# Performance work log

Measured on AMD Instinct MI355X. Metric: run time of the kernel, lower is better.

The kernel has to match this reference:

```python
import jax, jax.numpy as jnp
import numpy as np

HIDDEN = 256
HEADS = 8
HEAD_DIM = HIDDEN // HEADS
BATCH = 2
N_NODES = 8192
N_EDGES = 262144


def setup_inputs() -> dict:
    key = jax.random.key(0)
    ks = jax.random.split(key, 12)
    node_states = jax.random.normal(ks[0], (BATCH, N_NODES, HIDDEN), dtype=jnp.float32)
    b_idx = jax.random.randint(ks[1], (N_EDGES,), 0, BATCH)
    s_idx = jax.random.randint(ks[2], (N_EDGES,), 0, N_NODES)
    t_idx = jax.random.randint(ks[3], (N_EDGES,), 0, N_NODES)
    edge_indices = jnp.stack([b_idx, s_idx, t_idx]).astype(jnp.int64)
    edge_values = jax.random.normal(ks[4], (N_EDGES, HIDDEN), dtype=jnp.float32)
    scale = 1.0 / np.sqrt(HIDDEN)
    Wq = jax.random.normal(ks[5], (HIDDEN, HIDDEN), dtype=jnp.float32) * scale
    bq = jnp.zeros((HIDDEN,), jnp.float32)
    Wk = jax.random.normal(ks[6], (HIDDEN, HIDDEN), dtype=jnp.float32) * scale
    bk = jnp.zeros((HIDDEN,), jnp.float32)
    Wv = jax.random.normal(ks[7], (HIDDEN, HIDDEN), dtype=jnp.float32) * scale
    bv = jnp.zeros((HIDDEN,), jnp.float32)
    We = jax.random.normal(ks[8], (HIDDEN, HIDDEN), dtype=jnp.float32) * scale
    be = jnp.zeros((HIDDEN,), jnp.float32)
    return {"node_states": node_states, "edge_indices": edge_indices, "edge_values": edge_values,
            "Wq": Wq, "bq": bq, "Wk": Wk, "bk": bk, "Wv": Wv, "bv": bv, "We": We, "be": be}


def reference(node_states, edge_indices, edge_values, Wq, bq, Wk, bk, Wv, bv, We, be):
    batch, n_nodes, hidden = node_states.shape
    E = edge_indices.shape[1]
    b_idx, s_idx, t_idx = edge_indices[0], edge_indices[1], edge_indices[2]

    # Dense QKV projections over nodes (torch Linear: x @ W.T + b)
    Q = node_states @ Wq.T + bq
    K = node_states @ Wk.T + bk
    V = node_states @ Wv.T + bv

    # Gather per-edge query/key/value, split heads -> (E, H, D)
    Qm = Q[b_idx, s_idx].reshape(E, HEADS, HEAD_DIM)
    Kn = K[b_idx, t_idx].reshape(E, HEADS, HEAD_DIM)
    Vn = V[b_idx, t_idx].reshape(E, HEADS, HEAD_DIM)

    # Edge feature projections (use_edge_values=True path)
    Ke = (edge_values @ Wk.T + bk).reshape(E, HEADS, HEAD_DIM)
    Ve = (edge_values @ We.T + be).reshape(E, HEADS, HEAD_DIM)

    inv_sqrt_d = 1.0 / jnp.sqrt(jnp.float32(HEAD_DIM))
    # node2node + node2edge = Qm.(Kn+Ke)/sqrt(d)  -> (E, H)
    logits = jnp.sum(Qm * (Kn + Ke), axis=-1) * inv_sqrt_d

    # torch.sparse.softmax(..., dim=-1): dim -1 of (B,N,N,H) is the DENSE heads
    # dim, so softmax is taken over the heads axis of the per-edge values.
    attn = jax.nn.softmax(logits, axis=-1)  # (E, H)

    out_edges = (attn[..., None] * (Vn + Ve)).reshape(E, hidden)  # (E, hidden)

    # Scatter-sum edges to their (batch, src) node: sparse.mm with 0/1 mask
    seg = b_idx * n_nodes + s_idx
    flat = jax.ops.segment_sum(out_edges, seg, num_segments=batch * n_nodes)
    return flat.reshape(batch, n_nodes, hidden)
```

## Files before the change

### kernel.cpp

```cpp
#include <hip/hip_runtime.h>
#include <hip/hip_bf16.h>

#define HID 256
#define NN 8192
#define NE 262144

typedef float f32x4 __attribute__((ext_vector_type(4)));
typedef __bf16 bf16x8 __attribute__((ext_vector_type(8)));
typedef __bf16 bf16x4 __attribute__((ext_vector_type(4)));

__global__ void conv_weights(const float* __restrict__ wq, const float* __restrict__ wk,
                             const float* __restrict__ wv, const float* __restrict__ we,
                             __bf16* __restrict__ o) {
    int i = blockIdx.x * 256 + threadIdx.x;
    const float* srcs[4] = {wq, wk, wv, we};
    int m = i >> 16;
    int j = i & 65535;
    o[i] = (__bf16)srcs[m][j];
}

__global__ __launch_bounds__(256, 6)
void qkv_gemm(const float* __restrict__ x,
              const __bf16* __restrict__ wbf,
              const float* __restrict__ bq, const float* __restrict__ bk,
              const float* __restrict__ bv,
              __bf16* __restrict__ qbf, __bf16* __restrict__ kbf,
              __bf16* __restrict__ vbf) {
    __shared__ __bf16 xt[32 * 256];
    char* lb = (char*)xt;
    int tid = threadIdx.x;
    int blk = blockIdx.x;
    int m = blockIdx.y;

    const float4* xs = (const float4*)(x + (size_t)blk * 32 * 256);
    #pragma unroll
    for (int kq = 0; kq < 8; ++kq) {
        int f = tid + kq * 256;
        int row = f >> 6, c4 = f & 63;
        float4 v = xs[f];
        bf16x4 h;
        h[0] = (__bf16)v.x; h[1] = (__bf16)v.y; h[2] = (__bf16)v.z; h[3] = (__bf16)v.w;
        int off = (row * 512 + c4 * 8) ^ ((row & 7) << 4);
        *(bf16x4*)(lb + off) = h;
    }
    __syncthreads();

    int w = tid >> 6, lane = tid & 63;
    int l15 = lane & 15, l4 = lane >> 4;
    int cw = w * 64;
    const float* bias = (m == 0) ? bq : ((m == 1) ? bk : bv);
    __bf16* out = (m == 0) ? qbf : ((m == 1) ? kbf : vbf);

    const __bf16* W = wbf + (size_t)m * 65536;
    f32x4 acc[4][2] = {};
    for (int ks = 0; ks < 8; ++ks) {
        bf16x8 aW[4], bE[2];
        #pragma unroll
        for (int tn = 0; tn < 4; ++tn)
            aW[tn] = *(const bf16x8*)(W + (size_t)(cw + tn * 16 + l15) * 256 + ks * 32 + l4 * 8);
        #pragma unroll
        for (int te = 0; te < 2; ++te) {
            int row = te * 16 + l15;
            int off = (row * 512 + ks * 64 + l4 * 16) ^ ((row & 7) << 4);
            bE[te] = *(const bf16x8*)(lb + off);
        }
        #pragma unroll
        for (int tn = 0; tn < 4; ++tn)
            #pragma unroll
            for (int te = 0; te < 2; ++te)
                acc[tn][te] = __builtin_amdgcn_mfma_f32_16x16x32_bf16(aW[tn], bE[te], acc[tn][te], 0, 0, 0);
    }
    #pragma unroll
    for (int tn = 0; tn < 4; ++tn) {
        float4 b4 = *(const float4*)(bias + cw + tn * 16 + l4 * 4);
        #pragma unroll
        for (int te = 0; te < 2; ++te) {
            int row = blk * 32 + te * 16 + l15;
            int col = cw + tn * 16 + l4 * 4;
            bf16x4 h;
            h[0] = (__bf16)(acc[tn][te][0] + b4.x);
            h[1] = (__bf16)(acc[tn][te][1] + b4.y);
            h[2] = (__bf16)(acc[tn][te][2] + b4.z);
            h[3] = (__bf16)(acc[tn][te][3] + b4.w);
            *(bf16x4*)(out + (size_t)row * 256 + col) = h;
        }
    }
}

__global__ void k_hist(const int* __restrict__ eidx, unsigned* __restrict__ hist) {
    int e = blockIdx.x * 256 + threadIdx.x;
    int key = eidx[e] * NN + eidx[NE + e];
    atomicAdd(&hist[key], 1u);
}

__global__ void k_scan(const unsigned* __restrict__ hist, unsigned* __restrict__ cursor) {
    __shared__ unsigned tot[256];
    int tid = threadIdx.x;
    unsigned s = 0;
    for (int i = 0; i < 64; ++i) s += hist[tid * 64 + i];
    tot[tid] = s;
    __syncthreads();
    for (int d = 1; d < 256; d <<= 1) {
        unsigned v = (tid >= d) ? tot[tid - d] : 0u;
        __syncthreads();
        tot[tid] += v;
        __syncthreads();
    }
    unsigned run = (tid == 0) ? 0u : tot[tid - 1];
    for (int i = 0; i < 64; ++i) {
        int idx = tid * 64 + i;
        cursor[idx] = run;
        run += hist[idx];
    }
}

__global__ void k_perm(const int* __restrict__ eidx, unsigned* __restrict__ cursor,
                       int* __restrict__ perm) {
    int e = blockIdx.x * 256 + threadIdx.x;
    int key = eidx[e] * NN + eidx[NE + e];
    unsigned pos = atomicAdd(&cursor[key], 1u);
    perm[pos] = e;
}

__global__ __launch_bounds__(512, 8)
void edge_logits(const float* __restrict__ ev,
                 const int* __restrict__ eidx,
                 const __bf16* __restrict__ wbf,
                 const float* __restrict__ bkb,
                 const __bf16* __restrict__ qbf, const __bf16* __restrict__ kbf,
                 float* __restrict__ attn_ws) {
    __shared__ __bf16 evt[64 * 256];
    __shared__ int sb[64], ss[64], st[64];
    char* lb = (char*)evt;
    int tid = threadIdx.x;
    int e0 = blockIdx.x * 64;

    const float4* xs = (const float4*)(ev + (size_t)e0 * 256);
    #pragma unroll
    for (int kq = 0; kq < 8; ++kq) {
        int f = tid + kq * 512;
        int row = f >> 6, c4 = f & 63;
        float4 v = xs[f];
        bf16x4 h;
        h[0] = (__bf16)v.x; h[1] = (__bf16)v.y; h[2] = (__bf16)v.z; h[3] = (__bf16)v.w;
        int off = (row * 512 + c4 * 8) ^ ((row & 7) << 4);
        *(bf16x4*)(lb + off) = h;
    }
    if (tid < 64) {
        sb[tid] = eidx[e0 + tid];
        ss[tid] = eidx[NE + e0 + tid];
        st[tid] = eidx[2 * NE + e0 + tid];
    }
    __syncthreads();

    int w = tid >> 6, lane = tid & 63;
    int l15 = lane & 15, l4 = lane >> 4;
    int cw = w * 32;

    const __bf16* WK = wbf + 65536;
    f32x4 acc[2][4] = {};
    for (int ks = 0; ks < 8; ++ks) {
        bf16x8 aW[2], bE[4];
        #pragma unroll
        for (int tn = 0; tn < 2; ++tn)
            aW[tn] = *(const bf16x8*)(WK + (size_t)(cw + tn * 16 + l15) * 256 + ks * 32 + l4 * 8);
        #pragma unroll
        for (int te = 0; te < 4; ++te) {
            int row = te * 16 + l15;
            int off = (row * 512 + ks * 64 + l4 * 16) ^ ((row & 7) << 4);
            bE[te] = *(const bf16x8*)(lb + off);
        }
        #pragma unroll
        for (int tn = 0; tn < 2; ++tn)
            #pragma unroll
            for (int te = 0; te < 4; ++te)
                acc[tn][te] = __builtin_amdgcn_mfma_f32_16x16x32_bf16(aW[tn], bE[te], acc[tn][te], 0, 0, 0);
    }
    __syncthreads();

    #pragma unroll
    for (int tn = 0; tn < 2; ++tn) {
        float4 b4 = *(const float4*)(bkb + cw + tn * 16 + l4 * 4);
        #pragma unroll
        for (int te = 0; te < 4; ++te) {
            int edge = te * 16 + l15;
            int colb = (cw + tn * 16 + l4 * 4) * 2;
            bf16x4 h;
            h[0] = (__bf16)(acc[tn][te][0] + b4.x);
            h[1] = (__bf16)(acc[tn][te][1] + b4.y);
            h[2] = (__bf16)(acc[tn][te][2] + b4.z);
            h[3] = (__bf16)(acc[tn][te][3] + b4.w);
            int off = (edge * 512 + colb) ^ ((edge & 7) << 4);
            *(bf16x4*)(lb + off) = h;
        }
    }
    __syncthreads();

    int cl = lane & 31, eh = lane >> 5;
    #pragma unroll
    for (int it = 0; it < 4; ++it) {
        int e = w * 8 + it * 2 + eh;
        int b_ = sb[e], s_ = ss[e], t_ = st[e];
        bf16x8 qv = *(const bf16x8*)(qbf + ((size_t)b_ * NN + s_) * 256 + cl * 8);
        bf16x8 kv = *(const bf16x8*)(kbf + ((size_t)b_ * NN + t_) * 256 + cl * 8);
        int off = (e * 512 + cl * 16) ^ ((e & 7) << 4);
        bf16x8 kev = *(const bf16x8*)(lb + off);
        float val = 0.f;
        #pragma unroll
        for (int j = 0; j < 8; ++j)
            val += (float)qv[j] * ((float)kv[j] + (float)kev[j]);
        val += __shfl_xor(val, 1);
        val += __shfl_xor(val, 2);
        val *= 0.17677669529663687f;
        float mx = val;
        mx = fmaxf(mx, __shfl_xor(mx, 4));
        mx = fmaxf(mx, __shfl_xor(mx, 8));
        mx = fmaxf(mx, __shfl_xor(mx, 16));
        float ex = __expf(val - mx);
        float s4 = ex;
        s4 += __shfl_xor(s4, 4);
        s4 += __shfl_xor(s4, 8);
        s4 += __shfl_xor(s4, 16);
        float a = ex / s4;
        if ((cl & 3) == 0)
            attn_ws[(size_t)(e0 + e) * 8 + (cl >> 2)] = a;
    }
}

__global__ __launch_bounds__(512, 8)
void edge_scatter2(const float* __restrict__ ev,
                   const int* __restrict__ eidx,
                   const __bf16* __restrict__ wbf,
                   const float* __restrict__ beb,
                   const __bf16* __restrict__ vbf,
                   const float* __restrict__ attn_ws,
                   const int* __restrict__ perm,
                   float* __restrict__ out) {
    __shared__ __bf16 evt[64 * 256];
    __shared__ int pe[64], sb[64], ss[64], st[64];
    char* lb = (char*)evt;
    int tid = threadIdx.x;
    int p0 = blockIdx.x * 64;

    if (tid < 64) {
        int e = perm[p0 + tid];
        pe[tid] = e;
        sb[tid] = eidx[e];
        ss[tid] = eidx[NE + e];
        st[tid] = eidx[2 * NE + e];
    }
    __syncthreads();

    #pragma unroll
    for (int kq = 0; kq < 8; ++kq) {
        int f = tid + kq * 512;
        int row = f >> 6, c4 = f & 63;
        const float4* src = (const float4*)(ev + (size_t)pe[row] * 256);
        float4 v = src[c4];
        bf16x4 h;
        h[0] = (__bf16)v.x; h[1] = (__bf16)v.y; h[2] = (__bf16)v.z; h[3] = (__bf16)v.w;
        int off = (row * 512 + c4 * 8) ^ ((row & 7) << 4);
        *(bf16x4*)(lb + off) = h;
    }
    __syncthreads();

    int w = tid >> 6, lane = tid & 63;
    int l15 = lane & 15, l4 = lane >> 4;
    int cw = w * 32;

    const __bf16* WE = wbf + 3 * 65536;
    f32x4 acc[2][4] = {};
    for (int ks = 0; ks < 8; ++ks) {
        bf16x8 aW[2], bE[4];
        #pragma unroll
        for (int tn = 0; tn < 2; ++tn)
            aW[tn] = *(const bf16x8*)(WE + (size_t)(cw + tn * 16 + l15) * 256 + ks * 32 + l4 * 8);
        #pragma unroll
        for (int te = 0; te < 4; ++te) {
            int row = te * 16 + l15;
            int off = (row * 512 + ks * 64 + l4 * 16) ^ ((row & 7) << 4);
            bE[te] = *(const bf16x8*)(lb + off);
        }
        #pragma unroll
        for (int tn = 0; tn < 2; ++tn)
            #pragma unroll
            for (int te = 0; te < 4; ++te)
                acc[tn][te] = __builtin_amdgcn_mfma_f32_16x16x32_bf16(aW[tn], bE[te], acc[tn][te], 0, 0, 0);
    }
    __syncthreads();

    #pragma unroll
    for (int tn = 0; tn < 2; ++tn) {
        float4 b4 = *(const float4*)(beb + cw + tn * 16 + l4 * 4);
        #pragma unroll
        for (int te = 0; te < 4; ++te) {
            int edge = te * 16 + l15;
            int colb = (cw + tn * 16 + l4 * 4) * 2;
            bf16x4 h;
            h[0] = (__bf16)(acc[tn][te][0] + b4.x);
            h[1] = (__bf16)(acc[tn][te][1] + b4.y);
            h[2] = (__bf16)(acc[tn][te][2] + b4.z);
            h[3] = (__bf16)(acc[tn][te][3] + b4.w);
            int off = (edge * 512 + colb) ^ ((edge & 7) << 4);
            *(bf16x4*)(lb + off) = h;
        }
    }
    __syncthreads();

    float a0 = 0.f, a1 = 0.f, a2 = 0.f, a3 = 0.f;
    int havekey = -1;
    size_t obase = 0;
    #pragma unroll
    for (int it = 0; it < 8; ++it) {
        int e = w * 8 + it;
        int ge = pe[e];
        int b_ = sb[e], s_ = ss[e], t_ = st[e];
        const __bf16* vrow = vbf + ((size_t)b_ * NN + t_) * 256;
        const float* arow = attn_ws + (size_t)ge * 8;
        int swz = (e & 7) << 4;
        float c0, c1, c2, c3;
        {
            float att, vv, vev;
            int col, off;
            col = lane;             att = arow[0 + (lane >> 5)];
            vv = (float)vrow[col];  off = (e * 512 + col * 2) ^ swz;
            vev = (float)*(const __bf16*)(lb + off); c0 = att * (vv + vev);
            col = 64 + lane;        att = arow[2 + (lane >> 5)];
            vv = (float)vrow[col];  off = (e * 512 + col * 2) ^ swz;
            vev = (float)*(const __bf16*)(lb + off); c1 = att * (vv + vev);
            col = 128 + lane;       att = arow[4 + (lane >> 5)];
            vv = (float)vrow[col];  off = (e * 512 + col * 2) ^ swz;
            vev = (float)*(const __bf16*)(lb + off); c2 = att * (vv + vev);
            col = 192 + lane;       att = arow[6 + (lane >> 5)];
            vv = (float)vrow[col];  off = (e * 512 + col * 2) ^ swz;
            vev = (float)*(const __bf16*)(lb + off); c3 = att * (vv + vev);
        }
        int key = __builtin_amdgcn_readfirstlane(b_ * NN + s_);
        if (key != havekey) {
            if (havekey >= 0) {
                float* orow = out + obase;
                unsafeAtomicAdd(orow + lane, a0);
                unsafeAtomicAdd(orow + 64 + lane, a1);
                unsafeAtomicAdd(orow + 128 + lane, a2);
                unsafeAtomicAdd(orow + 192 + lane, a3);
            }
            a0 = c0; a1 = c1; a2 = c2; a3 = c3;
            havekey = key;
            obase = (size_t)key * 256;
        } else {
            a0 += c0; a1 += c1; a2 += c2; a3 += c3;
        }
    }
    if (havekey >= 0) {
        float* orow = out + obase;
        unsafeAtomicAdd(orow + lane, a0);
        unsafeAtomicAdd(orow + 64 + lane, a1);
        unsafeAtomicAdd(orow + 128 + lane, a2);
        unsafeAtomicAdd(orow + 192 + lane, a3);
    }
}

extern "C" void kernel_launch(void* const* d_in, const int* in_sizes, int n_in,
                              void* d_out, int out_size, void* d_ws, size_t ws_size,
                              hipStream_t stream) {
    const float* node_states = (const float*)d_in[0];
    const int*   eidx        = (const int*)d_in[1];
    const float* ev          = (const float*)d_in[2];
    const float* Wq          = (const float*)d_in[3];
    const float* bq          = (const float*)d_in[4];
    const float* Wk          = (const float*)d_in[5];
    const float* bk          = (const float*)d_in[6];
    const float* Wv          = (const float*)d_in[7];
    const float* bv          = (const float*)d_in[8];
    const float* We          = (const float*)d_in[9];
    const float* be          = (const float*)d_in[10];
    float* out = (float*)d_out;

    char* ws = (char*)d_ws;
    __bf16*   qbf     = (__bf16*)ws;
    __bf16*   kbf     = (__bf16*)(ws + 8388608);
    __bf16*   vbf     = (__bf16*)(ws + 16777216);
    float*    attn_ws = (float*)(ws + 25165824);
    __bf16*   wbf     = (__bf16*)(ws + 33554432);
    unsigned* hist    = (unsigned*)(ws + 34078720);
    unsigned* cursor  = (unsigned*)(ws + 34144256);
    int*      perm    = (int*)(ws + 34209792);

    hipMemsetAsync(d_out, 0, (size_t)out_size * sizeof(float), stream);
    hipMemsetAsync(hist, 0, 16384 * sizeof(unsigned), stream);
    conv_weights<<<1024, 256, 0, stream>>>(Wq, Wk, Wv, We, wbf);
    qkv_gemm<<<dim3(512, 3), 256, 0, stream>>>(node_states, wbf, bq, bk, bv, qbf, kbf, vbf);
    k_hist<<<1024, 256, 0, stream>>>(eidx, hist);
    k_scan<<<1, 256, 0, stream>>>(hist, cursor);
    k_perm<<<1024, 256, 0, stream>>>(eidx, cursor, perm);
    edge_logits<<<4096, 512, 0, stream>>>(ev, eidx, wbf, bk, qbf, kbf, attn_ws);
    edge_scatter2<<<4096, 512, 0, stream>>>(ev, eidx, wbf, be, vbf, attn_ws, perm, out);
}
```

Before: 326.0 us.

## Pre-convert edge values and node states to bf16 and read MFMA operands from global

Adds a conversion kernel that turns edge_values and node_states into bf16 buffers in the workspace once. The GEMM kernels then load B operands directly from global bf16 instead of staging fp32-to-bf16 tiles in LDS, and the loops are unrolled. The fp32 edge data used to be read twice (logits and scatter). Now it is read once, written once in bf16 and read twice at half size, and the LDS staging with its barriers is gone. The cost is an extra pass over 256MB of fp32 plus a 128MB bf16 write, and uncoalesced per-lane global operand loads.

```diff
diff --git a/kernel.cpp b/kernel.cpp
--- a/kernel.cpp
+++ b/kernel.cpp
@@ -19,31 +19,27 @@
     o[i] = (__bf16)srcs[m][j];
 }
 
-__global__ __launch_bounds__(256, 6)
-void qkv_gemm(const float* __restrict__ x,
+__global__ void conv_bf16(const float* __restrict__ in, __bf16* __restrict__ out, int n8) {
+    for (int i = blockIdx.x * 256 + threadIdx.x; i < n8; i += gridDim.x * 256) {
+        float4 a = ((const float4*)in)[i * 2];
+        float4 b = ((const float4*)in)[i * 2 + 1];
+        bf16x8 h;
+        h[0] = (__bf16)a.x; h[1] = (__bf16)a.y; h[2] = (__bf16)a.z; h[3] = (__bf16)a.w;
+        h[4] = (__bf16)b.x; h[5] = (__bf16)b.y; h[6] = (__bf16)b.z; h[7] = (__bf16)b.w;
+        ((bf16x8*)out)[i] = h;
+    }
+}
+
+__global__ __launch_bounds__(256, 4)
+void qkv_gemm(const __bf16* __restrict__ xb,
               const __bf16* __restrict__ wbf,
               const float* __restrict__ bq, const float* __restrict__ bk,
               const float* __restrict__ bv,
               __bf16* __restrict__ qbf, __bf16* __restrict__ kbf,
               __bf16* __restrict__ vbf) {
-    __shared__ __bf16 xt[32 * 256];
-    char* lb = (char*)xt;
     int tid = threadIdx.x;
     int blk = blockIdx.x;
     int m = blockIdx.y;
-
-    const float4* xs = (const float4*)(x + (size_t)blk * 32 * 256);
-    #pragma unroll
-    for (int kq = 0; kq < 8; ++kq) {
-        int f = tid + kq * 256;
-        int row = f >> 6, c4 = f & 63;
-        float4 v = xs[f];
-        bf16x4 h;
-        h[0] = (__bf16)v.x; h[1] = (__bf16)v.y; h[2] = (__bf16)v.z; h[3] = (__bf16)v.w;
-        int off = (row * 512 + c4 * 8) ^ ((row & 7) << 4);
-        *(bf16x4*)(lb + off) = h;
-    }
-    __syncthreads();
 
     int w = tid >> 6, lane = tid & 63;
     int l15 = lane & 15, l4 = lane >> 4;
@@ -53,17 +49,15 @@
 
     const __bf16* W = wbf + (size_t)m * 65536;
     f32x4 acc[4][2] = {};
+    #pragma unroll
     for (int ks = 0; ks < 8; ++ks) {
         bf16x8 aW[4], bE[2];
         #pragma unroll
         for (int tn = 0; tn < 4; ++tn)
             aW[tn] = *(const bf16x8*)(W + (size_t)(cw + tn * 16 + l15) * 256 + ks * 32 + l4 * 8);
         #pragma unroll
-        for (int te = 0; te < 2; ++te) {
-            int row = te * 16 + l15;
-            int off = (row * 512 + ks * 64 + l4 * 16) ^ ((row & 7) << 4);
-            bE[te] = *(const bf16x8*)(lb + off);
-        }
+        for (int te = 0; te < 2; ++te)
+            bE[te] = *(const bf16x8*)(xb + (size_t)(blk * 32 + te * 16 + l15) * 256 + ks * 32 + l4 * 8);
         #pragma unroll
         for (int tn = 0; tn < 4; ++tn)
             #pragma unroll
@@ -122,36 +116,24 @@
     perm[pos] = e;
 }
 
-__global__ __launch_bounds__(512, 8)
-void edge_logits(const float* __restrict__ ev,
+__global__ __launch_bounds__(512, 4)
+void edge_logits(const __bf16* __restrict__ evb,
                  const int* __restrict__ eidx,
                  const __bf16* __restrict__ wbf,
                  const float* __restrict__ bkb,
                  const __bf16* __restrict__ qbf, const __bf16* __restrict__ kbf,
                  float* __restrict__ attn_ws) {
-    __shared__ __bf16 evt[64 * 256];
+    __shared__ __bf16 ket[64 * 256];
     __shared__ int sb[64], ss[64], st[64];
-    char* lb = (char*)evt;
+    char* lb = (char*)ket;
     int tid = threadIdx.x;
     int e0 = blockIdx.x * 64;
 
-    const float4* xs = (const float4*)(ev + (size_t)e0 * 256);
-    #pragma unroll
-    for (int kq = 0; kq < 8; ++kq) {
-        int f = tid + kq * 512;
-        int row = f >> 6, c4 = f & 63;
-        float4 v = xs[f];
-        bf16x4 h;
-        h[0] = (__bf16)v.x; h[1] = (__bf16)v.y; h[2] = (__bf16)v.z; h[3] = (__bf16)v.w;
-        int off = (row * 512 + c4 * 8) ^ ((row & 7) << 4);
-        *(bf16x4*)(lb + off) = h;
-    }
     if (tid < 64) {
         sb[tid] = eidx[e0 + tid];
         ss[tid] = eidx[NE + e0 + tid];
         st[tid] = eidx[2 * NE + e0 + tid];
     }
-    __syncthreads();
 
     int w = tid >> 6, lane = tid & 63;
     int l15 = lane & 15, l4 = lane >> 4;
@@ -159,24 +141,21 @@
 
     const __bf16* WK = wbf + 65536;
     f32x4 acc[2][4] = {};
+    #pragma unroll
     for (int ks = 0; ks < 8; ++ks) {
         bf16x8 aW[2], bE[4];
         #pragma unroll
         for (int tn = 0; tn < 2; ++tn)
             aW[tn] = *(const bf16x8*)(WK + (size_t)(cw + tn * 16 + l15) * 256 + ks * 32 + l4 * 8);
         #pragma unroll
-        for (int te = 0; te < 4; ++te) {
-            int row = te * 16 + l15;
-            int off = (row * 512 + ks * 64 + l4 * 16) ^ ((row & 7) << 4);
-            bE[te] = *(const bf16x8*)(lb + off);
-        }
+        for (int te = 0; te < 4; ++te)
+            bE[te] = *(const bf16x8*)(evb + (size_t)(e0 + te * 16 + l15) * 256 + ks * 32 + l4 * 8);
         #pragma unroll
         for (int tn = 0; tn < 2; ++tn)
             #pragma unroll
             for (int te = 0; te < 4; ++te)
                 acc[tn][te] = __builtin_amdgcn_mfma_f32_16x16x32_bf16(aW[tn], bE[te], acc[tn][te], 0, 0, 0);
     }
-    __syncthreads();
 
     #pragma unroll
     for (int tn = 0; tn < 2; ++tn) {
@@ -227,8 +206,8 @@
     }
 }
 
-__global__ __launch_bounds__(512, 8)
-void edge_scatter2(const float* __restrict__ ev,
+__global__ __launch_bounds__(512, 4)
+void edge_scatter2(const __bf16* __restrict__ evb,
                    const int* __restrict__ eidx,
                    const __bf16* __restrict__ wbf,
                    const float* __restrict__ beb,
@@ -236,9 +215,9 @@
                    const float* __restrict__ attn_ws,
                    const int* __restrict__ perm,
                    float* __restrict__ out) {
-    __shared__ __bf16 evt[64 * 256];
+    __shared__ __bf16 vet[64 * 256];
     __shared__ int pe[64], sb[64], ss[64], st[64];
-    char* lb = (char*)evt;
+    char* lb = (char*)vet;
     int tid = threadIdx.x;
     int p0 = blockIdx.x * 64;
 
@@ -251,43 +230,27 @@
     }
     __syncthreads();
 
-    #pragma unroll
-    for (int kq = 0; kq < 8; ++kq) {
-        int f = tid + kq * 512;
-        int row = f >> 6, c4 = f & 63;
-        const float4* src = (const float4*)(ev + (size_t)pe[row] * 256);
-        float4 v = src[c4];
-        bf16x4 h;
-        h[0] = (__bf16)v.x; h[1] = (__bf16)v.y; h[2] = (__bf16)v.z; h[3] = (__bf16)v.w;
-        int off = (row * 512 + c4 * 8) ^ ((row & 7) << 4);
-        *(bf16x4*)(lb + off) = h;
-    }
-    __syncthreads();
-
     int w = tid >> 6, lane = tid & 63;
     int l15 = lane & 15, l4 = lane >> 4;
     int cw = w * 32;
 
     const __bf16* WE = wbf + 3 * 65536;
     f32x4 acc[2][4] = {};
+    #pragma unroll
     for (int ks = 0; ks < 8; ++ks) {
         bf16x8 aW[2], bE[4];
         #pragma unroll
         for (int tn = 0; tn < 2; ++tn)
             aW[tn] = *(const bf16x8*)(WE + (size_t)(cw + tn * 16 + l15) * 256 + ks * 32 + l4 * 8);
         #pragma unroll
-        for (int te = 0; te < 4; ++te) {
-            int row = te * 16 + l15;
-            int off = (row * 512 + ks * 64 + l4 * 16) ^ ((row & 7) << 4);
-            bE[te] = *(const bf16x8*)(lb + off);
-        }
+        for (int te = 0; te < 4; ++te)
+            bE[te] = *(const bf16x8*)(evb + (size_t)pe[te * 16 + l15] * 256 + ks * 32 + l4 * 8);
         #pragma unroll
         for (int tn = 0; tn < 2; ++tn)
             #pragma unroll
             for (int te = 0; te < 4; ++te)
                 acc[tn][te] = __builtin_amdgcn_mfma_f32_16x16x32_bf16(aW[tn], bE[te], acc[tn][te], 0, 0, 0);
     }
-    __syncthreads();
 
     #pragma unroll
     for (int tn = 0; tn < 2; ++tn) {
@@ -385,14 +348,18 @@
     unsigned* hist    = (unsigned*)(ws + 34078720);
     unsigned* cursor  = (unsigned*)(ws + 34144256);
     int*      perm    = (int*)(ws + 34209792);
+    __bf16*   evb     = (__bf16*)(ws + 35258368);
+    __bf16*   xb      = (__bf16*)(ws + 169476096);
 
     hipMemsetAsync(d_out, 0, (size_t)out_size * sizeof(float), stream);
     hipMemsetAsync(hist, 0, 16384 * sizeof(unsigned), stream);
     conv_weights<<<1024, 256, 0, stream>>>(Wq, Wk, Wv, We, wbf);
-    qkv_gemm<<<dim3(512, 3), 256, 0, stream>>>(node_states, wbf, bq, bk, bv, qbf, kbf, vbf);
+    conv_bf16<<<4096, 256, 0, stream>>>(ev, evb, NE * 256 / 8);
+    conv_bf16<<<2048, 256, 0, stream>>>(node_states, xb, 2 * NN * 256 / 8);
+    qkv_gemm<<<dim3(512, 3), 256, 0, stream>>>(xb, wbf, bq, bk, bv, qbf, kbf, vbf);
     k_hist<<<1024, 256, 0, stream>>>(eidx, hist);
     k_scan<<<1, 256, 0, stream>>>(hist, cursor);
     k_perm<<<1024, 256, 0, stream>>>(eidx, cursor, perm);
-    edge_logits<<<4096, 512, 0, stream>>>(ev, eidx, wbf, bk, qbf, kbf, attn_ws);
-    edge_scatter2<<<4096, 512, 0, stream>>>(ev, eidx, wbf, be, vbf, attn_ws, perm, out);
-}
+    edge_logits<<<4096, 512, 0, stream>>>(evb, eidx, wbf, bk, qbf, kbf, attn_ws);
+    edge_scatter2<<<4096, 512, 0, stream>>>(evb, eidx, wbf, be, vbf, attn_ws, perm, out);
+}
```

Result: slower. 552.5 us (+69.5%).
